# Optimization experiments

Hardware: AMD Instinct MI355X
Metric: run time of the kernel (lower is better)

Reference implementation:

```python
import jax, jax.numpy as jnp
import numpy as np


def conv2d(x, w, b, pad):
    # NCHW conv, stride 1, symmetric padding
    out = jax.lax.conv_general_dilated(
        x, w, window_strides=(1, 1), padding=[(pad, pad), (pad, pad)],
        dimension_numbers=("NCHW", "OIHW", "NCHW"))
    return out + b[None, :, None, None]


def setup_inputs() -> dict:
    key = jax.random.key(0)
    ks = jax.random.split(key, 18)
    B, C, H, W = 4, 256, 64, 64
    Cq = C // 16  # 16
    Ck = C // 8   # 32
    s = 0.02
    return {
        "x": jax.random.normal(ks[0], (B, C, H, W), jnp.float32),
        "dw1_w": jax.random.normal(ks[1], (Cq, C, 7, 7), jnp.float32) * s,
        "dw1_b": jnp.zeros((Cq,), jnp.float32),
        "dw2_w": jax.random.normal(ks[2], (Cq, C, 11, 11), jnp.float32) * s,
        "dw2_b": jnp.zeros((Cq,), jnp.float32),
        "key_w": jax.random.normal(ks[3], (Ck, C, 1, 1), jnp.float32) * s,
        "key_b": jnp.zeros((Ck,), jnp.float32),
        "value_w": jax.random.normal(ks[4], (C, C, 1, 1), jnp.float32) * s,
        "value_b": jnp.zeros((C,), jnp.float32),
        "conv1_w": jax.random.normal(ks[5], (Cq, C, 3, 3), jnp.float32) * s,
        "conv1_b": jnp.zeros((Cq,), jnp.float32),
        "conv2_w": jax.random.normal(ks[6], (C, Cq, 3, 3), jnp.float32) * s,
        "conv2_b": jnp.zeros((C,), jnp.float32),
        "se_w": jax.random.normal(ks[7], (C, C, 1, 1), jnp.float32) * s,
        "se_b": jnp.zeros((C,), jnp.float32),
        "gamma1": jnp.zeros((1,), jnp.float32) + 0.1,  # nonzero so attention path is exercised
        "gamma2": jnp.zeros((1,), jnp.float32) + 0.1,
    }


def reference(x, dw1_w, dw1_b, dw2_w, dw2_b, key_w, key_b, value_w, value_b,
              conv1_w, conv1_b, conv2_w, conv2_b, se_w, se_b, gamma1, gamma2):
    B, C, H, W = x.shape
    HW = H * W
    # q: concat of 7x7 and 11x11 conv branches -> (B, HW, C//8)
    q = jnp.concatenate([conv2d(x, dw1_w, dw1_b, 3), conv2d(x, dw2_w, dw2_b, 5)], axis=1)
    q = q.reshape(B, -1, HW).transpose(0, 2, 1)
    # k: 1x1 conv -> (B, C//8, HW)
    k = conv2d(x, key_w, key_b, 0).reshape(B, -1, HW)
    # raw (unscaled) full spatial attention, softmax over last dim
    att = jax.nn.softmax(jnp.einsum("bnc,bcm->bnm", q, k), axis=-1)  # (B, HW, HW)
    v = conv2d(x, value_w, value_b, 0).reshape(B, C, HW)
    out = jnp.einsum("bcm,bnm->bcn", v, att).reshape(B, C, H, W)
    # local conv branch + channel attention (SE)
    y = conv2d(jax.nn.silu(conv2d(x, conv1_w, conv1_b, 1)), conv2_w, conv2_b, 1)
    pooled = jnp.mean(y, axis=(2, 3), keepdims=True)  # (B, C, 1, 1)
    se = y * jax.nn.sigmoid(conv2d(pooled, se_w, se_b, 0))
    return gamma1 * out + gamma2 * se + x
```

## Files before the change

### kernel.cpp

```cpp
#include <hip/hip_runtime.h>

typedef unsigned short u16;
typedef __bf16 bf16x8 __attribute__((ext_vector_type(8)));
typedef float f32x4 __attribute__((ext_vector_type(4)));
typedef float f32x16 __attribute__((ext_vector_type(16)));

#define MFMA16(A,B,C) __builtin_amdgcn_mfma_f32_16x16x32_bf16((A),(B),(C),0,0,0)
#define MFMA32(A,B,C) __builtin_amdgcn_mfma_f32_32x32x16_bf16((A),(B),(C),0,0,0)

__device__ __forceinline__ u16 f2b(float f){
  union { float f; unsigned u; } X; X.f = f;
  unsigned r = X.u + 0x7FFFu + ((X.u >> 16) & 1u);
  return (u16)(r >> 16);
}
__device__ __forceinline__ float b2f(u16 h){
  union { unsigned u; float f; } X; X.u = ((unsigned)h) << 16; return X.f;
}
__device__ __forceinline__ unsigned pack2(float lo, float hi){
  union { float f; unsigned u; } L, H; L.f = lo; H.f = hi;
  return (H.u & 0xFFFF0000u) | (L.u >> 16);
}
__device__ __forceinline__ bf16x8 ld_frag(const u16* p){
  union { uint4 u; bf16x8 v; } U; U.u = *(const uint4*)p; return U.v;
}

__global__ __launch_bounds__(256) void k_prep_w(
    const float* __restrict__ dw1, const float* __restrict__ dw2,
    const float* __restrict__ cw1, const float* __restrict__ kw,
    const float* __restrict__ vw,  const float* __restrict__ cw2,
    u16* __restrict__ wB, u16* __restrict__ wC,
    u16* __restrict__ kwt, u16* __restrict__ vwt, u16* __restrict__ w2t){
  int i = blockIdx.x * 256 + threadIdx.x;
  const int NB = 991232, NC = 73728, NK = 8192, NV = 65536, N2 = 40960;
  if(i < NB){
    int tap = i >> 13, rem = i & 8191;
    int chunk = rem >> 9, r2 = rem & 511;
    int oc = r2 >> 4, ci = chunk*16 + (r2 & 15);
    int dy = tap / 11, dx = tap - dy*11;
    float v;
    if(oc < 16){
      v = (dy >= 2 && dy <= 8 && dx >= 2 && dx <= 8) ? dw1[(oc*256 + ci)*49 + (dy-2)*7 + (dx-2)] : 0.f;
    } else {
      v = dw2[((oc-16)*256 + ci)*121 + tap];
    }
    wB[i] = f2b(v);
    return;
  }
  i -= NB;
  if(i < NC){
    int tap = i >> 13, rem = i & 8191;
    int chunk = rem >> 9, r2 = rem & 511;
    int oc = r2 >> 4, ci = chunk*16 + (r2 & 15);
    wC[i] = (oc < 16) ? f2b(cw1[(oc*256 + ci)*9 + tap]) : (u16)0;
    return;
  }
  i -= NC;
  if(i < NK){ kwt[i] = f2b(kw[i]); return; }
  i -= NK;
  if(i < NV){ vwt[i] = f2b(vw[i]); return; }
  i -= NV;
  if(i < N2){
    int co = i/160, kk = i - co*160;
    int tap = kk >> 4, ci = kk & 15;
    w2t[i] = (tap < 9) ? f2b(cw2[co*144 + ci*9 + tap]) : (u16)0;
    return;
  }
}

__global__ __launch_bounds__(256) void k_prep_x(const float* __restrict__ x, u16* __restrict__ xp){
  __shared__ float tile[32][33];
  const int bid = blockIdx.x;
  const int b = bid >> 10, rem = bid & 1023;
  const int c0 = (rem >> 7) << 5, m0 = (rem & 127) << 5;
  const int t = threadIdx.x;
  { const int cg = t >> 5, mm = t & 31;
    #pragma unroll
    for(int i=0;i<4;i++)
      tile[cg*4+i][mm] = x[((size_t)(b*256 + c0 + cg*4 + i) << 12) + m0 + mm];
  }
  __syncthreads();
  { const int cp = (t & 15) << 1, mloc = t >> 4;
    #pragma unroll
    for(int half = 0; half < 2; ++half){
      const int ml = half*16 + mloc;
      const int m = m0 + ml;
      const int yy = (m >> 6) + 5, xx = (m & 63) + 5;
      const int ci = c0 + cp;
      const int chunk = ci >> 4, wi = ci & 15;
      u16 lo = f2b(tile[cp][ml]), hi = f2b(tile[cp+1][ml]);
      *(unsigned*)&xp[(((size_t)(b*16 + chunk)*74 + yy)*80 + xx)*16 + wi] = ((unsigned)hi << 16) | lo;
    }
  }
}

__global__ __launch_bounds__(256) void k_qconv(
    const u16* __restrict__ xp, const u16* __restrict__ wB, const u16* __restrict__ wC,
    u16* __restrict__ qp){
  __shared__ __align__(16) u16 buf[15360];
  const int bid = blockIdx.x;
  const int rg = bid & 31, b = (bid >> 5) & 3, kq = bid >> 7;
  const int y0 = rg << 1;
  const int t = threadIdx.x, wv = t >> 6, lane = t & 63;
  const int m = lane & 31, kh = lane >> 5;
  const int laneoff = m*16 + kh*8;
  const int r = wv & 1, xo = (wv >> 1) << 5;
  const f32x16 z16 = {0.f,0.f,0.f,0.f,0.f,0.f,0.f,0.f,0.f,0.f,0.f,0.f,0.f,0.f,0.f,0.f};
  f32x16 acc = z16, acc1 = z16;

  #pragma unroll 1
  for(int c = 0; c < 2; ++c){
    const int chunk = kq*2 + c;
    const uint4* src = (const uint4*)(xp + ((size_t)((b*16 + chunk)*74 + y0))*1280);
    __syncthreads();
    for(int e = t; e < 1920; e += 256){
      ((uint4*)buf)[(e & 1)*960 + (e >> 1)] = src[e];
    }
    __syncthreads();
    const u16* wBc = wB + chunk*512 + laneoff;
    const u16* wCc = wC + chunk*512 + laneoff;
    const u16* ap = buf + kh*7680 + (r*80 + xo + m)*8;
    #pragma unroll 1
    for(int dy = 0; dy < 11; ++dy){
      const u16* rowp = ap + dy*640;
      const u16* wrow = wBc + dy*11*8192;
      const bool in1y = (dy >= 4) & (dy <= 6);
      #pragma unroll
      for(int dx = 0; dx < 11; ++dx){
        bf16x8 A = ld_frag(rowp + dx*8);
        bf16x8 B = ld_frag(wrow + dx*8192);
        acc = MFMA32(A, B, acc);
        if(in1y && dx >= 4 && dx <= 6){
          bf16x8 B1 = ld_frag(wCc + ((dy-4)*3 + (dx-4))*8192);
          acc1 = MFMA32(A, B1, acc1);
        }
      }
    }
  }

  u16* qb = qp + ((size_t)kq*16384 + (b << 12) + (y0 + r)*64 + xo) * 48;
  #pragma unroll
  for(int reg = 0; reg < 16; ++reg){
    const int row = (reg & 3) + ((reg >> 2) << 3) + (kh << 2);
    qb[row*48 + m] = f2b(acc[reg]);
    if(m < 16) qb[row*48 + 32 + m] = f2b(acc1[reg]);
  }
}

__global__ __launch_bounds__(256) void k_qfin(
    const u16* __restrict__ qp, const float* __restrict__ b7,
    const float* __restrict__ b11, const float* __restrict__ b1,
    u16* __restrict__ q_t, u16* __restrict__ t1){
  const int t = threadIdx.x, wv = t >> 6, lane = t & 63;
  const int px = blockIdx.x*4 + wv;
  if(lane >= 48) return;
  const size_t off = (size_t)px*48 + lane;
  float s = 0.f;
  #pragma unroll
  for(int sp = 0; sp < 8; ++sp) s += b2f(qp[off + (size_t)sp*786432]);
  const float LOG2E = 1.44269504f;
  if(lane < 16){
    q_t[px*32 + lane] = f2b((s + b7[lane]) * LOG2E);
  } else if(lane < 32){
    q_t[px*32 + lane] = f2b((s + b11[lane - 16]) * LOG2E);
  } else {
    float v = s + b1[lane - 32];
    t1[px*16 + lane - 32] = f2b(v / (1.f + __expf(-v)));
  }
}

__global__ __launch_bounds__(256) void k_kv(
    const u16* __restrict__ xp, const u16* __restrict__ vwt, const u16* __restrict__ kwt,
    const float* __restrict__ vb, const float* __restrict__ kb,
    u16* __restrict__ vt, u16* __restrict__ k_t){
  const int bid = blockIdx.x;
  const int h = bid & 3, blk = (bid >> 2) & 63, b = bid >> 8;
  const int wv = threadIdx.x >> 6, lane = threadIdx.x & 63;
  const int col = lane & 15, quad = lane >> 4;
  const int m0 = (blk << 6) + (wv << 4);
  f32x4 z = {0.f,0.f,0.f,0.f};
  f32x4 av[4], ak[2];
  #pragma unroll
  for(int i=0;i<4;i++) av[i] = z;
  ak[0] = z; ak[1] = z;
  const int m = m0 + col;
  const int py = (m >> 6) + 5, pxx = (m & 63) + 5;
  #pragma unroll 1
  for(int ch = 0; ch < 8; ++ch){
    const int cio = ch*32 + quad*8;
    const int chunk = cio >> 4, wi = cio & 15;
    bf16x8 xf = ld_frag(xp + (((size_t)(b*16 + chunk)*74 + py)*80 + pxx)*16 + wi);
    #pragma unroll
    for(int ct2 = 0; ct2 < 4; ++ct2){
      bf16x8 wf = ld_frag(vwt + (((h*4 + ct2)*16 + col) << 8) + cio);
      av[ct2] = MFMA16(wf, xf, av[ct2]);
    }
    if(h == 0){
      #pragma unroll
      for(int kt = 0; kt < 2; ++kt){
        bf16x8 kf = ld_frag(kwt + ((kt*16 + col) << 8) + cio);
        ak[kt] = MFMA16(xf, kf, ak[kt]);
      }
    }
  }
  const int g = m0 >> 5, lo = (m0 & 31) + col;
  #pragma unroll
  for(int ct2 = 0; ct2 < 4; ++ct2){
    #pragma unroll
    for(int r = 0; r < 4; ++r){
      const int c = (h*4 + ct2)*16 + quad*4 + r;
      vt[((size_t)(b*128 + g)*256 + c)*32 + lo] = f2b(av[ct2][r] + vb[c]);
    }
  }
  if(h == 0){
    #pragma unroll
    for(int kt = 0; kt < 2; ++kt){
      #pragma unroll
      for(int r = 0; r < 4; ++r){
        const int mq = b*4096 + m0 + quad*4 + r;
        k_t[mq*32 + kt*16 + col] = f2b((ak[kt][r] + kb[kt*16 + col]) );
      }
    }
  }
}

__global__ __launch_bounds__(512) void k_attn(
    const u16* __restrict__ q_t, const u16* __restrict__ k_t,
    const u16* __restrict__ vt, u16* __restrict__ Op,
    float* __restrict__ lsav){
  __shared__ __align__(16) float S[128][68];
  __shared__ __align__(16) u16 P[128][72];
  __shared__ float l_l[128];
  const int bid = blockIdx.x;
  const int q0 = (bid & 31) << 7, b = (bid >> 5) & 3, ks = bid >> 7;
  const int t = threadIdx.x, wv = t >> 6, lane = t & 63, col = lane & 15, quad = lane >> 4;
  const int qp2 = wv & 3, kh2 = wv >> 2;
  const int cb = wv << 5;
  const int sr = t >> 2, sc = t & 3;
  const bf16x8 qf0 = ld_frag(q_t + (size_t)(b*4096 + q0 + (qp2*2+0)*16 + col) * 32 + quad*8);
  const bf16x8 qf1 = ld_frag(q_t + (size_t)(b*4096 + q0 + (qp2*2+1)*16 + col) * 32 + quad*8);
  const f32x4 z = {0.f,0.f,0.f,0.f};
  f32x4 acc[8][2];
  #pragma unroll
  for(int qq=0;qq<8;qq++){ acc[qq][0] = z; acc[qq][1] = z; }
  float l_i = 0.f;
  const u16* kbase = k_t + (size_t)(b*4096) * 32;
  const u16* vbase = vt + (size_t)(b*128) * 8192;

  auto QK = [&](int kt){
    const int mm0 = kt << 6;
    #pragma unroll
    for(int ki = 0; ki < 2; ++ki){
      bf16x8 kf = ld_frag(kbase + (size_t)(mm0 + (kh2*2+ki)*16 + col) * 32 + quad*8);
      const int cc2 = (kh2*2+ki)*16 + col;
      f32x4 s0 = MFMA16(qf0, kf, z);
      f32x4 s1 = MFMA16(qf1, kf, z);
      const int r0 = (qp2*2+0)*16 + quad*4, r1 = (qp2*2+1)*16 + quad*4;
      S[r0+0][cc2] = s0[0]; S[r0+1][cc2] = s0[1]; S[r0+2][cc2] = s0[2]; S[r0+3][cc2] = s0[3];
      S[r1+0][cc2] = s1[0]; S[r1+1][cc2] = s1[1]; S[r1+2][cc2] = s1[2]; S[r1+3][cc2] = s1[3];
    }
  };

  const int ktEnd = ks*16 + 16;
  QK(ks*16);
  for(int kt = ks*16; kt < ktEnd; ++kt){
    __syncthreads();
    {
      const float* srow = &S[sr][sc*16];
      float4 s0 = *(const float4*)(srow);
      float4 s1 = *(const float4*)(srow + 4);
      float4 s2 = *(const float4*)(srow + 8);
      float4 s3 = *(const float4*)(srow + 12);
      float p0 = exp2f(s0.x), p1 = exp2f(s0.y), p2 = exp2f(s0.z), p3 = exp2f(s0.w);
      float p4 = exp2f(s1.x), p5 = exp2f(s1.y), p6 = exp2f(s1.z), p7 = exp2f(s1.w);
      float p8 = exp2f(s2.x), p9 = exp2f(s2.y), pa = exp2f(s2.z), pb = exp2f(s2.w);
      float pc = exp2f(s3.x), pd = exp2f(s3.y), pe = exp2f(s3.z), pf = exp2f(s3.w);
      float sum = (((p0+p1)+(p2+p3)) + ((p4+p5)+(p6+p7)))
                + (((p8+p9)+(pa+pb)) + ((pc+pd)+(pe+pf)));
      sum += __shfl_xor(sum,1); sum += __shfl_xor(sum,2);
      l_i += sum;
      uint4 w0, w1;
      w0.x = pack2(p0,p1); w0.y = pack2(p2,p3); w0.z = pack2(p4,p5); w0.w = pack2(p6,p7);
      w1.x = pack2(p8,p9); w1.y = pack2(pa,pb); w1.z = pack2(pc,pd); w1.w = pack2(pe,pf);
      *(uint4*)&P[sr][sc*16] = w0;
      *(uint4*)&P[sr][sc*16 + 8] = w1;
    }
    __syncthreads();
    {
      bf16x8 vf[2][2];
      #pragma unroll
      for(int ct = 0; ct < 2; ++ct)
        #pragma unroll
        for(int chh = 0; chh < 2; ++chh)
          vf[ct][chh] = ld_frag(vbase + ((size_t)(kt*2 + chh)*256 + cb + ct*16 + col)*32 + quad*8);
      #pragma unroll
      for(int qq = 0; qq < 8; ++qq){
        bf16x8 pa0 = ld_frag(&P[qq*16 + col][quad*8]);
        bf16x8 pa1 = ld_frag(&P[qq*16 + col][32 + quad*8]);
        acc[qq][0] = MFMA16(pa0, vf[0][0], acc[qq][0]);
        acc[qq][1] = MFMA16(pa0, vf[1][0], acc[qq][1]);
        acc[qq][0] = MFMA16(pa1, vf[0][1], acc[qq][0]);
        acc[qq][1] = MFMA16(pa1, vf[1][1], acc[qq][1]);
      }
    }
    if(kt + 1 < ktEnd) QK(kt + 1);
  }
  if(sc == 0){
    l_l[sr] = l_i;
    lsav[ks*16384 + b*4096 + q0 + sr] = l_i;
  }
  __syncthreads();
  #pragma unroll
  for(int qq = 0; qq < 8; ++qq){
    #pragma unroll
    for(int r = 0; r < 4; ++r){
      const float inv = 1.f / l_l[qq*16 + quad*4 + r];
      const int n = q0 + qq*16 + quad*4 + r;
      u16* orow = Op + ((size_t)(ks*16384 + b*4096 + n) << 8) + cb + col;
      orow[0]  = f2b(acc[qq][0][r] * inv);
      orow[16] = f2b(acc[qq][1][r] * inv);
    }
  }
}

__global__ __launch_bounds__(256) void k_conv2(
    const u16* __restrict__ t1, const u16* __restrict__ w2t, const float* __restrict__ b2,
    u16* __restrict__ y_t, float* __restrict__ pooled){
  __shared__ __align__(16) u16 im[64][168];
  __shared__ float pool_l[64];
  const int bid = blockIdx.x;
  const int h = bid & 3, y = (bid >> 2) & 63, b = bid >> 8;
  const int t = threadIdx.x;
  if(t < 64) pool_l[t] = 0.f;
  const u16* t1b = t1 + ((size_t)(b*4096) << 4);
  {
    const int px = t >> 2, ci0 = (t & 3) << 2;
    #pragma unroll
    for(int tap = 0; tap < 9; ++tap){
      const int ky = (tap*11) >> 5, kx = tap - ky*3;
      const int ryy = y + ky - 1, rxx = px + kx - 1;
      uint2 val = make_uint2(0u, 0u);
      if((unsigned)ryy < 64u && (unsigned)rxx < 64u)
        val = *(const uint2*)(t1b + (((ryy << 6) + rxx) << 4) + ci0);
      *(uint2*)&im[px][tap*16 + ci0] = val;
    }
    for(int e = t; e < 1024; e += 256){ im[e >> 4][144 + (e & 15)] = 0; }
  }
  __syncthreads();
  const int wv = t >> 6, lane = t & 63, col = lane & 15, quad = lane >> 4;
  const f32x4 z = {0.f,0.f,0.f,0.f};
  f32x4 acc[4];
  #pragma unroll
  for(int i=0;i<4;i++) acc[i] = z;
  #pragma unroll
  for(int ch = 0; ch < 5; ++ch){
    bf16x8 af = ld_frag(&im[wv*16 + col][ch*32 + quad*8]);
    #pragma unroll
    for(int j = 0; j < 4; ++j){
      bf16x8 wf = ld_frag(w2t + ((h*4 + j)*16 + col)*160 + ch*32 + quad*8);
      acc[j] = MFMA16(af, wf, acc[j]);
    }
  }
  const int m0 = (y << 6) + (wv << 4) + (quad << 2);
  #pragma unroll
  for(int j = 0; j < 4; ++j){
    const int c = (h*4 + j)*16 + col;
    const float bias = b2[c];
    float s = 0.f;
    #pragma unroll
    for(int r = 0; r < 4; ++r){
      float v = acc[j][r] + bias;
      y_t[((size_t)(b*4096 + m0 + r) << 8) + c] = f2b(v);
      s += v;
    }
    s += __shfl_xor(s, 16); s += __shfl_xor(s, 32);
    if(quad == 0) atomicAdd(&pool_l[c - h*64], s);
  }
  __syncthreads();
  if(t < 64) atomicAdd(&pooled[b*256 + h*64 + t], pool_l[t]);
}

__global__ __launch_bounds__(256) void k_final(
    const u16* __restrict__ Op, const u16* __restrict__ y_t, const float* __restrict__ x,
    const float* __restrict__ lsav, const float* __restrict__ pooled,
    const float* __restrict__ sew, const float* __restrict__ seb,
    const float* __restrict__ g1p, const float* __restrict__ g2p,
    float* __restrict__ out){
  __shared__ float tO[32][65];
  __shared__ float tY[32][65];
  __shared__ float gate_l[32];
  const int bid = blockIdx.x;
  const int b = bid >> 9, rem = bid & 511;
  const int c0 = (rem >> 6) << 5, m0 = (rem & 63) << 6;
  const int t = threadIdx.x;
  const float g1 = g1p[0], g2 = g2p[0];
  {
    const int cl = t >> 3, k0 = (t & 7) << 5;
    const int c = c0 + cl;
    const float* wr = sew + (size_t)c*256 + k0;
    const float* pr = pooled + b*256 + k0;
    float part = 0.f;
    #pragma unroll
    for(int j = 0; j < 32; j += 4){
      float4 w4 = *(const float4*)(wr + j);
      float4 p4 = *(const float4*)(pr + j);
      part += w4.x*p4.x + w4.y*p4.y + w4.z*p4.z + w4.w*p4.w;
    }
    part += __shfl_xor(part, 1); part += __shfl_xor(part, 2); part += __shfl_xor(part, 4);
    if((t & 7) == 0){
      float a = part * (1.f/4096.f) + seb[c];
      gate_l[cl] = g2 / (1.f + __expf(-a));
    }
  }
  { const int ml = t >> 2, cg = (t & 3) << 3;
    const int gq = b*4096 + m0 + ml;
    const float l0 = lsav[gq], l1 = lsav[16384 + gq], l2 = lsav[32768 + gq], l3 = lsav[49152 + gq];
    const float inv = 1.f / (l0 + l1 + l2 + l3);
    const float w0 = l0*inv, w1 = l1*inv, w2 = l2*inv, w3 = l3*inv;
    const size_t base = ((size_t)gq << 8) + c0 + cg;
    union { uint4 u; u16 s[8]; } A0, A1, A2, A3;
    A0.u = *(const uint4*)(Op + base);
    A1.u = *(const uint4*)(Op + base + ((size_t)16384 << 8));
    A2.u = *(const uint4*)(Op + base + ((size_t)32768 << 8));
    A3.u = *(const uint4*)(Op + base + ((size_t)49152 << 8));
    #pragma unroll
    for(int i = 0; i < 8; ++i)
      tO[cg+i][ml] = w0*b2f(A0.s[i]) + w1*b2f(A1.s[i]) + w2*b2f(A2.s[i]) + w3*b2f(A3.s[i]);
    const u16* yrow = y_t + base;
    uint4 yu = *(const uint4*)yrow;
    tY[cg+0][ml]=b2f((u16)(yu.x & 0xffffu)); tY[cg+1][ml]=b2f((u16)(yu.x >> 16));
    tY[cg+2][ml]=b2f((u16)(yu.y & 0xffffu)); tY[cg+3][ml]=b2f((u16)(yu.y >> 16));
    tY[cg+4][ml]=b2f((u16)(yu.z & 0xffffu)); tY[cg+5][ml]=b2f((u16)(yu.z >> 16));
    tY[cg+6][ml]=b2f((u16)(yu.w & 0xffffu)); tY[cg+7][ml]=b2f((u16)(yu.w >> 16));
  }
  __syncthreads();
  { const int cl = t >> 3, mg = (t & 7) << 3;
    const int c = c0 + cl;
    const float gate = gate_l[cl];
    const float* xrow = x + ((size_t)(b*256 + c) << 12) + m0 + mg;
    float* orow = out + ((size_t)(b*256 + c) << 12) + m0 + mg;
    float4 x0 = *(const float4*)xrow, x1 = *(const float4*)(xrow + 4);
    float4 r0, r1;
    r0.x = g1*tO[cl][mg+0] + gate*tY[cl][mg+0] + x0.x;
    r0.y = g1*tO[cl][mg+1] + gate*tY[cl][mg+1] + x0.y;
    r0.z = g1*tO[cl][mg+2] + gate*tY[cl][mg+2] + x0.z;
    r0.w = g1*tO[cl][mg+3] + gate*tY[cl][mg+3] + x0.w;
    r1.x = g1*tO[cl][mg+4] + gate*tY[cl][mg+4] + x1.x;
    r1.y = g1*tO[cl][mg+5] + gate*tY[cl][mg+5] + x1.y;
    r1.z = g1*tO[cl][mg+6] + gate*tY[cl][mg+6] + x1.z;
    r1.w = g1*tO[cl][mg+7] + gate*tY[cl][mg+7] + x1.w;
    *(float4*)orow = r0;
    *(float4*)(orow + 4) = r1;
  }
}

extern "C" void kernel_launch(void* const* d_in, const int* in_sizes, int n_in,
                              void* d_out, int out_size, void* d_ws, size_t ws_size,
                              hipStream_t stream){
  (void)in_sizes; (void)n_in; (void)out_size; (void)ws_size;
  const float* x    = (const float*)d_in[0];
  const float* dw1w = (const float*)d_in[1];
  const float* dw1b = (const float*)d_in[2];
  const float* dw2w = (const float*)d_in[3];
  const float* dw2b = (const float*)d_in[4];
  const float* keyw = (const float*)d_in[5];
  const float* keyb = (const float*)d_in[6];
  const float* valw = (const float*)d_in[7];
  const float* valb = (const float*)d_in[8];
  const float* c1w  = (const float*)d_in[9];
  const float* c1b  = (const float*)d_in[10];
  const float* c2w  = (const float*)d_in[11];
  const float* c2b  = (const float*)d_in[12];
  const float* sew  = (const float*)d_in[13];
  const float* seb  = (const float*)d_in[14];
  const float* g1   = (const float*)d_in[15];
  const float* g2   = (const float*)d_in[16];
  float* out = (float*)d_out;

  char* w = (char*)d_ws;
  auto take = [&](size_t bytes) -> char* {
    char* p = w; w += (bytes + 255) & ~(size_t)255; return p;
  };
  u16*  Op   = (u16*)  take(33554432);
  u16*  q_t  = (u16*)  take(1048576);
  u16*  k_t  = (u16*)  take(1048576);
  u16*  vt   = (u16*)  take(8388608);
  u16*  t1   = (u16*)  take(524288);
  u16*  y_t  = (u16*)  take(8388608);
  u16*  kwt  = (u16*)  take(16384);
  u16*  vwt  = (u16*)  take(131072);
  u16*  w2t  = (u16*)  take(81920);
  float* pooled = (float*)take(4096);
  float* lsav   = (float*)take(262144);

  u16*  xp = Op;
  u16*  qp = Op + 6062080;
  u16*  wB = vt;
  u16*  wC = vt + 991232;

  hipMemsetAsync(xp, 0, 12124160, stream);
  hipMemsetAsync(pooled, 0, 4096, stream);
  k_prep_w<<<4608, 256, 0, stream>>>(dw1w, dw2w, c1w, keyw, valw, c2w, wB, wC, kwt, vwt, w2t);
  k_prep_x<<<4096, 256, 0, stream>>>(x, xp);
  k_qconv<<<1024, 256, 0, stream>>>(xp, wB, wC, qp);
  k_qfin<<<4096, 256, 0, stream>>>(qp, dw1b, dw2b, c1b, q_t, t1);
  k_kv<<<1024, 256, 0, stream>>>(xp, vwt, kwt, valb, keyb, vt, k_t);
  k_attn<<<512, 512, 0, stream>>>(q_t, k_t, vt, Op, lsav);
  k_conv2<<<1024, 256, 0, stream>>>(t1, w2t, c2b, y_t, pooled);
  k_final<<<2048, 256, 0, stream>>>(Op, y_t, x, lsav, pooled, sew, seb, g1, g2, out);
}
```

Baseline: 284.0 us.

## Fuse exp into QK MFMA epilogue with double-buffered P tile in attention

```diff
diff --git a/kernel.cpp b/kernel.cpp
--- a/kernel.cpp
+++ b/kernel.cpp
@@ -16,9 +16,9 @@
 __device__ __forceinline__ float b2f(u16 h){
   union { unsigned u; float f; } X; X.u = ((unsigned)h) << 16; return X.f;
 }
-__device__ __forceinline__ unsigned pack2(float lo, float hi){
-  union { float f; unsigned u; } L, H; L.f = lo; H.f = hi;
-  return (H.u & 0xFFFF0000u) | (L.u >> 16);
+__device__ __forceinline__ u16 f2b_trunc(float f){
+  union { float f; unsigned u; } X; X.f = f;
+  return (u16)(X.u >> 16);
 }
 __device__ __forceinline__ bf16x8 ld_frag(const u16* p){
   union { uint4 u; bf16x8 v; } U; U.u = *(const uint4*)p; return U.v;
@@ -227,62 +227,44 @@
     const u16* __restrict__ q_t, const u16* __restrict__ k_t,
     const u16* __restrict__ vt, u16* __restrict__ Op,
     float* __restrict__ lsav){
-  __shared__ __align__(16) float S[128][68];
-  __shared__ __align__(16) u16 P[128][72];
+  __shared__ __align__(16) u16 P[2][128][72];
+  __shared__ float lred[2][128];
   __shared__ float l_l[128];
   const int bid = blockIdx.x;
   const int q0 = (bid & 31) << 7, b = (bid >> 5) & 3, ks = bid >> 7;
   const int t = threadIdx.x, wv = t >> 6, lane = t & 63, col = lane & 15, quad = lane >> 4;
   const int qp2 = wv & 3, kh2 = wv >> 2;
   const int cb = wv << 5;
-  const int sr = t >> 2, sc = t & 3;
   const bf16x8 qf0 = ld_frag(q_t + (size_t)(b*4096 + q0 + (qp2*2+0)*16 + col) * 32 + quad*8);
   const bf16x8 qf1 = ld_frag(q_t + (size_t)(b*4096 + q0 + (qp2*2+1)*16 + col) * 32 + quad*8);
   const f32x4 z = {0.f,0.f,0.f,0.f};
   f32x4 acc[8][2];
   #pragma unroll
   for(int qq=0;qq<8;qq++){ acc[qq][0] = z; acc[qq][1] = z; }
-  float l_i = 0.f;
+  float lp0[4] = {0.f,0.f,0.f,0.f};
+  float lp1[4] = {0.f,0.f,0.f,0.f};
   const u16* kbase = k_t + (size_t)(b*4096) * 32;
   const u16* vbase = vt + (size_t)(b*128) * 8192;
 
-  auto QK = [&](int kt){
+  const int ktEnd = ks*16 + 16;
+  for(int kt = ks*16; kt < ktEnd; ++kt){
+    const int pb = kt & 1;
     const int mm0 = kt << 6;
-    #pragma unroll
-    for(int ki = 0; ki < 2; ++ki){
-      bf16x8 kf = ld_frag(kbase + (size_t)(mm0 + (kh2*2+ki)*16 + col) * 32 + quad*8);
-      const int cc2 = (kh2*2+ki)*16 + col;
-      f32x4 s0 = MFMA16(qf0, kf, z);
-      f32x4 s1 = MFMA16(qf1, kf, z);
-      const int r0 = (qp2*2+0)*16 + quad*4, r1 = (qp2*2+1)*16 + quad*4;
-      S[r0+0][cc2] = s0[0]; S[r0+1][cc2] = s0[1]; S[r0+2][cc2] = s0[2]; S[r0+3][cc2] = s0[3];
-      S[r1+0][cc2] = s1[0]; S[r1+1][cc2] = s1[1]; S[r1+2][cc2] = s1[2]; S[r1+3][cc2] = s1[3];
-    }
-  };
-
-  const int ktEnd = ks*16 + 16;
-  QK(ks*16);
-  for(int kt = ks*16; kt < ktEnd; ++kt){
-    __syncthreads();
     {
-      const float* srow = &S[sr][sc*16];
-      float4 s0 = *(const float4*)(srow);
-      float4 s1 = *(const float4*)(srow + 4);
-      float4 s2 = *(const float4*)(srow + 8);
-      float4 s3 = *(const float4*)(srow + 12);
-      float p0 = exp2f(s0.x), p1 = exp2f(s0.y), p2 = exp2f(s0.z), p3 = exp2f(s0.w);
-      float p4 = exp2f(s1.x), p5 = exp2f(s1.y), p6 = exp2f(s1.z), p7 = exp2f(s1.w);
-      float p8 = exp2f(s2.x), p9 = exp2f(s2.y), pa = exp2f(s2.z), pb = exp2f(s2.w);
-      float pc = exp2f(s3.x), pd = exp2f(s3.y), pe = exp2f(s3.z), pf = exp2f(s3.w);
-      float sum = (((p0+p1)+(p2+p3)) + ((p4+p5)+(p6+p7)))
-                + (((p8+p9)+(pa+pb)) + ((pc+pd)+(pe+pf)));
-      sum += __shfl_xor(sum,1); sum += __shfl_xor(sum,2);
-      l_i += sum;
-      uint4 w0, w1;
-      w0.x = pack2(p0,p1); w0.y = pack2(p2,p3); w0.z = pack2(p4,p5); w0.w = pack2(p6,p7);
-      w1.x = pack2(p8,p9); w1.y = pack2(pa,pb); w1.z = pack2(pc,pd); w1.w = pack2(pe,pf);
-      *(uint4*)&P[sr][sc*16] = w0;
-      *(uint4*)&P[sr][sc*16 + 8] = w1;
+      #pragma unroll
+      for(int ki = 0; ki < 2; ++ki){
+        bf16x8 kf = ld_frag(kbase + (size_t)(mm0 + (kh2*2+ki)*16 + col) * 32 + quad*8);
+        f32x4 s0 = MFMA16(qf0, kf, z);
+        f32x4 s1 = MFMA16(qf1, kf, z);
+        const int cc = (kh2*2+ki)*16 + col;
+        u16* P0 = &P[pb][(qp2*2+0)*16 + quad*4][cc];
+        u16* P1 = &P[pb][(qp2*2+1)*16 + quad*4][cc];
+        #pragma unroll
+        for(int r = 0; r < 4; ++r){
+          float p0 = exp2f(s0[r]); lp0[r] += p0; P0[r*72] = f2b_trunc(p0);
+          float p1 = exp2f(s1[r]); lp1[r] += p1; P1[r*72] = f2b_trunc(p1);
+        }
+      }
     }
     __syncthreads();
     {
@@ -294,19 +276,34 @@
           vf[ct][chh] = ld_frag(vbase + ((size_t)(kt*2 + chh)*256 + cb + ct*16 + col)*32 + quad*8);
       #pragma unroll
       for(int qq = 0; qq < 8; ++qq){
-        bf16x8 pa0 = ld_frag(&P[qq*16 + col][quad*8]);
-        bf16x8 pa1 = ld_frag(&P[qq*16 + col][32 + quad*8]);
+        bf16x8 pa0 = ld_frag(&P[pb][qq*16 + col][quad*8]);
+        bf16x8 pa1 = ld_frag(&P[pb][qq*16 + col][32 + quad*8]);
         acc[qq][0] = MFMA16(pa0, vf[0][0], acc[qq][0]);
         acc[qq][1] = MFMA16(pa0, vf[1][0], acc[qq][1]);
         acc[qq][0] = MFMA16(pa1, vf[0][1], acc[qq][0]);
         acc[qq][1] = MFMA16(pa1, vf[1][1], acc[qq][1]);
       }
     }
-    if(kt + 1 < ktEnd) QK(kt + 1);
-  }
-  if(sc == 0){
-    l_l[sr] = l_i;
-    lsav[ks*16384 + b*4096 + q0 + sr] = l_i;
+  }
+  #pragma unroll
+  for(int r = 0; r < 4; ++r){
+    lp0[r] += __shfl_xor(lp0[r],1); lp0[r] += __shfl_xor(lp0[r],2);
+    lp0[r] += __shfl_xor(lp0[r],4); lp0[r] += __shfl_xor(lp0[r],8);
+    lp1[r] += __shfl_xor(lp1[r],1); lp1[r] += __shfl_xor(lp1[r],2);
+    lp1[r] += __shfl_xor(lp1[r],4); lp1[r] += __shfl_xor(lp1[r],8);
+  }
+  if(col == 0){
+    #pragma unroll
+    for(int r = 0; r < 4; ++r){
+      lred[kh2][(qp2*2+0)*16 + quad*4 + r] = lp0[r];
+      lred[kh2][(qp2*2+1)*16 + quad*4 + r] = lp1[r];
+    }
+  }
+  __syncthreads();
+  if(t < 128){
+    const float L = lred[0][t] + lred[1][t];
+    l_l[t] = L;
+    lsav[ks*16384 + b*4096 + q0 + t] = L;
   }
   __syncthreads();
   #pragma unroll
@@ -332,8 +329,7 @@
   const int t = threadIdx.x;
   if(t < 64) pool_l[t] = 0.f;
   const u16* t1b = t1 + ((size_t)(b*4096) << 4);
-  {
-    const int px = t >> 2, ci0 = (t & 3) << 2;
+  { const int px = t >> 2, ci0 = (t & 3) << 2;
     #pragma unroll
     for(int tap = 0; tap < 9; ++tap){
       const int ky = (tap*11) >> 5, kx = tap - ky*3;
@@ -393,8 +389,7 @@
   const int c0 = (rem >> 6) << 5, m0 = (rem & 63) << 6;
   const int t = threadIdx.x;
   const float g1 = g1p[0], g2 = g2p[0];
-  {
-    const int cl = t >> 3, k0 = (t & 7) << 5;
+  { const int cl = t >> 3, k0 = (t & 7) << 5;
     const int c = c0 + cl;
     const float* wr = sew + (size_t)c*256 + k0;
     const float* pr = pooled + b*256 + k0;
```

Result: no change. 281.7 us (-0.8%).
